# Optimization experiments

Measured on AMD Instinct MI355X. Metric: run time of the kernel, lower is better.

## Reference

```python
import jax, jax.numpy as jnp
import numpy as np

B, DIM, HEADS, HD, H, W = 1, 256, 8, 32, 64, 64
MLP = int(DIM * 4.0)
EPS = 1e-5


def _ln(x, g, b):
    # LayerNorm over channel dim of NCHW (torch applies it on NHWC last dim)
    mu = x.mean(axis=1, keepdims=True)
    var = ((x - mu) ** 2).mean(axis=1, keepdims=True)
    return (x - mu) / jnp.sqrt(var + EPS) * g[None, :, None, None] + b[None, :, None, None]


def _c1(x, w, b):
    # 1x1 conv: w is [out, in]
    return jnp.einsum('bchw,oc->bohw', x, w) + b[None, :, None, None]


def _c3(x, w, b):
    y = jax.lax.conv_general_dilated(x, w, (1, 1), ((1, 1), (1, 1)),
                                     dimension_numbers=('NCHW', 'OIHW', 'NCHW'))
    return y + b[None, :, None, None]


def setup_inputs() -> dict:
    key = jax.random.key(0)
    ks = jax.random.split(key, 16)
    init = lambda k, s: jax.random.normal(k, s, jnp.float32) * 0.02
    d = {}
    d['rgb_feat'] = jax.random.normal(ks[0], (B, DIM, H, W), jnp.float32)
    d['dpt_feat'] = jax.random.normal(ks[1], (B, DIM, H, W), jnp.float32)
    d['x_dpt'] = jax.random.normal(ks[2], (B, 1, 1024, 1024), jnp.float32)
    d['wq'] = init(ks[3], (DIM, DIM)); d['bq'] = jnp.zeros((DIM,), jnp.float32)
    d['wk'] = init(ks[4], (DIM, DIM)); d['bk'] = jnp.zeros((DIM,), jnp.float32)
    d['wv'] = init(ks[5], (DIM, DIM)); d['bv'] = jnp.zeros((DIM,), jnp.float32)
    d['wo'] = init(ks[6], (DIM, DIM)); d['bo'] = jnp.zeros((DIM,), jnp.float32)
    d['g_rgb'] = jnp.ones((DIM,), jnp.float32); d['b_rgb'] = jnp.zeros((DIM,), jnp.float32)
    d['g_dpt'] = jnp.ones((DIM,), jnp.float32); d['b_dpt'] = jnp.zeros((DIM,), jnp.float32)
    d['g1'] = jnp.ones((DIM,), jnp.float32); d['b1'] = jnp.zeros((DIM,), jnp.float32)
    d['g2'] = jnp.ones((DIM,), jnp.float32); d['b2'] = jnp.zeros((DIM,), jnp.float32)
    d['w_mlp1'] = init(ks[7], (MLP, DIM)); d['b_mlp1'] = jnp.zeros((MLP,), jnp.float32)
    d['w_mlp2'] = init(ks[8], (DIM, MLP)); d['b_mlp2'] = jnp.zeros((DIM,), jnp.float32)
    d['w_de1'] = init(ks[9], (DIM, 1, 3, 3)); d['b_de1'] = jnp.zeros((DIM,), jnp.float32)
    d['w_de2'] = init(ks[10], (DIM, DIM)); d['b_de2'] = jnp.zeros((DIM,), jnp.float32)
    d['pos_emb'] = init(ks[11], (1, DIM, 1, 1))
    d['scale'] = jnp.sqrt(jnp.float32(HD))
    return d


def reference(rgb_feat, dpt_feat, x_dpt, wq, bq, wk, bk, wv, bv, wo, bo,
              g_rgb, b_rgb, g_dpt, b_dpt, g1, b1, g2, b2,
              w_mlp1, b_mlp1, w_mlp2, b_mlp2, w_de1, b_de1, w_de2, b_de2,
              pos_emb, scale):
    Bn, C, Hh, Ww = rgb_feat.shape
    n = Hh * Ww
    rgb_ln = _ln(rgb_feat, g_rgb, b_rgb)
    dpt_ln = _ln(dpt_feat, g_dpt, b_dpt)
    # depth positional embedding: bilinear downsample (align_corners=False) + conv3x3 + relu + conv1x1
    xd = jax.image.resize(x_dpt, (Bn, 1, Hh, Ww), method='bilinear', antialias=False)
    pe = _c1(jax.nn.relu(_c3(xd, w_de1, b_de1)), w_de2, b_de2)
    rgb_ln = rgb_ln + pos_emb + pe
    dpt_ln = dpt_ln + pos_emb + pe
    # QKV as [B, heads, head_dim, N]
    q = _c1(rgb_ln, wq, bq).reshape(Bn, HEADS, HD, n)
    k = _c1(dpt_ln, wk, bk).reshape(Bn, HEADS, HD, n)
    v = _c1(dpt_ln, wv, bv).reshape(Bn, HEADS, HD, n)
    scores = jnp.einsum('bhdn,bhdm->bhnm', q, k) / scale
    attn = jax.nn.softmax(scores, axis=-1)  # dropout is identity in eval
    fused = jnp.einsum('bhnm,bhdm->bhdn', attn, v).reshape(Bn, C, Hh, Ww)
    out = _c1(fused, wo, bo) + rgb_feat
    out_ln = _ln(out, g1, b1)
    h = jax.nn.gelu(_c1(out_ln, w_mlp1, b_mlp1), approximate=False)
    mlp_out = _c1(h, w_mlp2, b_mlp2)
    out2 = mlp_out + out_ln
    return _ln(out2, g2, b2)
```

## Files before the change

### kernel.cpp

```cpp
#include <hip/hip_runtime.h>
#include <hip/hip_bf16.h>
#include <math.h>

constexpr int NTOK = 4096;
constexpr int CDIM = 256;
constexpr int MLPD = 1024;
constexpr float EPS_LN = 1e-5f;

typedef __attribute__((ext_vector_type(8))) short bf16x8;
typedef __attribute__((ext_vector_type(4))) float floatx4;
typedef __attribute__((ext_vector_type(16))) float f32x16;
typedef __attribute__((ext_vector_type(2))) unsigned int u32x2;
typedef unsigned short u16;
typedef unsigned int u32;

#if defined(__has_builtin)
#if __has_builtin(__builtin_amdgcn_permlane32_swap)
#define HAVE_PLSWAP 1
#endif
#endif

__device__ __forceinline__ u16 f2bf(float x) {
    union { float f; u32 u; } v; v.f = x;
    u32 r = v.u + 0x7fff + ((v.u >> 16) & 1);
    return (u16)(r >> 16);
}
__device__ __forceinline__ float bf2f(u16 u) {
    union { u32 i; float f; } v; v.i = ((u32)u) << 16; return v.f;
}
__device__ __forceinline__ u32 pkbf(float a, float b) {
    __hip_bfloat162 h = __float22bfloat162_rn(make_float2(a, b));
    union { __hip_bfloat162 h; u32 u; } v; v.h = h; return v.u;
}
__device__ __forceinline__ float gelu_exact(float x) {
    return 0.5f * x * (1.0f + erff(x * 0.70710678118654752f));
}

__global__ __launch_bounds__(256) void k_prep(const float* __restrict__ rgb,
                                              float* __restrict__ rgbT,
                                              const float* __restrict__ dpt,
                                              float* __restrict__ dptT,
                                              const float* __restrict__ xdpt,
                                              const float* __restrict__ w3,
                                              const float* __restrict__ b3,
                                              u16* __restrict__ y,
                                              const float* __restrict__ wq,
                                              const float* __restrict__ wk,
                                              const float* __restrict__ wv,
                                              const float* __restrict__ wo,
                                              const float* __restrict__ wde2,
                                              const float* __restrict__ wm1,
                                              const float* __restrict__ wm2,
                                              u16* __restrict__ arena) {
    int blk = blockIdx.x;
    int t = threadIdx.x;
    if (blk < 512) {
        const float* in = (blk < 256) ? rgb : dpt;
        float* out = (blk < 256) ? rgbT : dptT;
        int tb = blk & 255;
        int c0 = (tb & 63) * 64, r0 = (tb >> 6) * 64;
        __shared__ float T[64][65];
        int rr = t >> 4, cc = (t & 15) * 4;
#pragma unroll
        for (int i = 0; i < 4; ++i) {
            int row = i * 16 + rr;
            float4 v = *(const float4*)(in + (size_t)(r0 + row) * NTOK + c0 + cc);
            T[row][cc] = v.x; T[row][cc + 1] = v.y; T[row][cc + 2] = v.z; T[row][cc + 3] = v.w;
        }
        __syncthreads();
#pragma unroll
        for (int i = 0; i < 4; ++i) {
            int a = i * 16 + rr;
            float4 v;
            v.x = T[cc][a]; v.y = T[cc + 1][a]; v.z = T[cc + 2][a]; v.w = T[cc + 3][a];
            *(float4*)(out + (size_t)(c0 + a) * CDIM + r0 + cc) = v;
        }
    } else if (blk < 768) {
        __shared__ float nb[3][18];
        int n0 = (blk - 512) * 16;
        int yy = n0 >> 6, x0 = n0 & 63;
        if (t < 54) {
            int r = t / 18, cc = t % 18;
            int sy = yy - 1 + r, sx = x0 - 1 + cc;
            float v = 0.f;
            if (sy >= 0 && sy < 64 && sx >= 0 && sx < 64) {
                int r0 = 16 * sy + 7, c0 = 16 * sx + 7;
                v = 0.25f * (xdpt[r0 * 1024 + c0] + xdpt[r0 * 1024 + c0 + 1] +
                             xdpt[(r0 + 1) * 1024 + c0] + xdpt[(r0 + 1) * 1024 + c0 + 1]);
            }
            nb[r][cc] = v;
        }
        __syncthreads();
        float wv9[9];
#pragma unroll
        for (int i = 0; i < 9; ++i) wv9[i] = w3[t * 9 + i];
        float bb = b3[t];
#pragma unroll
        for (int k = 0; k < 16; ++k) {
            float acc = bb;
#pragma unroll
            for (int r = 0; r < 3; ++r)
#pragma unroll
                for (int kx = 0; kx < 3; ++kx) acc += wv9[r * 3 + kx] * nb[r][k + kx];
            y[(size_t)(n0 + k) * CDIM + t] = f2bf(fmaxf(acc, 0.f));
        }
    } else {
        int e0 = (blk - 768) * 1024 + t * 4;
        const float* src; int off;
        if (e0 < 65536)       { src = wq;   off = 0; }
        else if (e0 < 131072) { src = wk;   off = 65536; }
        else if (e0 < 196608) { src = wv;   off = 131072; }
        else if (e0 < 262144) { src = wo;   off = 196608; }
        else if (e0 < 327680) { src = wde2; off = 262144; }
        else if (e0 < 589824) { src = wm1;  off = 327680; }
        else                  { src = wm2;  off = 589824; }
        float4 v = *(const float4*)(src + (e0 - off));
        uint2 o; o.x = pkbf(v.x, v.y); o.y = pkbf(v.z, v.w);
        *(uint2*)(arena + e0) = o;
    }
}

__global__ __launch_bounds__(256) void k_lnT(const void* __restrict__ xA,
                                             const float* __restrict__ gA,
                                             const float* __restrict__ bA,
                                             void* __restrict__ yA,
                                             const void* __restrict__ xB,
                                             const float* __restrict__ gB,
                                             const float* __restrict__ bB,
                                             void* __restrict__ yB,
                                             const u16* __restrict__ pe,
                                             const float* __restrict__ pos,
                                             int xf32) {
    const void* x; const float* g; const float* bb; void* y;
    if (blockIdx.y == 0) { x = xA; g = gA; bb = bA; y = yA; }
    else                 { x = xB; g = gB; bb = bB; y = yB; }
    int n = blockIdx.x * 4 + (threadIdx.x >> 6);
    int lane = threadIdx.x & 63;
    int c = lane * 4;
    float4 xv;
    if (xf32) {
        xv = *((const float4*)x + (size_t)n * 64 + lane);
    } else {
        ushort4 u = *((const ushort4*)x + (size_t)n * 64 + lane);
        xv = make_float4(bf2f(u.x), bf2f(u.y), bf2f(u.z), bf2f(u.w));
    }
    float s = xv.x + xv.y + xv.z + xv.w;
    float s2 = xv.x * xv.x + xv.y * xv.y + xv.z * xv.z + xv.w * xv.w;
#pragma unroll
    for (int off = 1; off < 64; off <<= 1) {
        s += __shfl_xor(s, off, 64);
        s2 += __shfl_xor(s2, off, 64);
    }
    float mu = s * (1.0f / 256.0f);
    float var = s2 * (1.0f / 256.0f) - mu * mu;
    float rsd = rsqrtf(var + EPS_LN);
    float4 g4 = *(const float4*)(g + c);
    float4 b4 = *(const float4*)(bb + c);
    float4 o;
    o.x = (xv.x - mu) * rsd * g4.x + b4.x;
    o.y = (xv.y - mu) * rsd * g4.y + b4.y;
    o.z = (xv.z - mu) * rsd * g4.z + b4.z;
    o.w = (xv.w - mu) * rsd * g4.w + b4.w;
    if (pe) {
        float4 p4 = *(const float4*)(pos + c);
        ushort4 pu = *((const ushort4*)pe + (size_t)n * 64 + lane);
        o.x += p4.x + bf2f(pu.x);
        o.y += p4.y + bf2f(pu.y);
        o.z += p4.z + bf2f(pu.z);
        o.w += p4.w + bf2f(pu.w);
    }
    ushort4 ou;
    ou.x = f2bf(o.x); ou.y = f2bf(o.y); ou.z = f2bf(o.z); ou.w = f2bf(o.w);
    *((ushort4*)y + (size_t)n * 64 + lane) = ou;
}

#define LDB 72
__global__ __launch_bounds__(512) void k_bmm(const u16* __restrict__ X0, const void* __restrict__ W0,
                                             const float* __restrict__ B0, void* __restrict__ Y0, int f0,
                                             const u16* __restrict__ X1, const void* __restrict__ W1,
                                             const float* __restrict__ B1, void* __restrict__ Y1, int f1,
                                             const u16* __restrict__ X2, const void* __restrict__ W2,
                                             const float* __restrict__ B2, void* __restrict__ Y2, int f2,
                                             const void* __restrict__ res, const float* __restrict__ scl,
                                             int M, int K) {
    const u16* X; const void* Wp; const float* bias; void* Yp; int flags;
    if (blockIdx.z == 0)      { X = X0; Wp = W0; bias = B0; Yp = Y0; flags = f0; }
    else if (blockIdx.z == 1) { X = X1; Wp = W1; bias = B1; Yp = Y1; flags = f1; }
    else                      { X = X2; Wp = W2; bias = B2; Yp = Y2; flags = f2; }
    __shared__ u16 Xs[2][64 * LDB];
    __shared__ u16 Ws[2][64 * LDB];
    float* Cred = (float*)&Xs[0][0];

    int tid = threadIdx.x;
    int kg = tid >> 8;
    int t = tid & 255;
    int wid = t >> 6, lane = t & 63;
    int lo16 = lane & 15, quad = lane >> 4;
    int wy = wid & 1, wx = wid >> 1;
    int n0 = blockIdx.x * 64, m0 = blockIdx.y * 64;
    int srow = t >> 2, sseg = t & 3;
    int Khalf = K >> 1;
    int kbase = kg * Khalf;

    floatx4 acc[2][2];
#pragma unroll
    for (int i = 0; i < 2; ++i)
#pragma unroll
        for (int j = 0; j < 2; ++j) acc[i][j] = floatx4{0.f, 0.f, 0.f, 0.f};

    for (int k0 = 0; k0 < Khalf; k0 += 64) {
        int kk = kbase + k0;
        const u16* xp = X + (size_t)(n0 + srow) * K + kk + sseg * 16;
        uint4 xr0 = *(const uint4*)xp;
        uint4 xr1 = *(const uint4*)(xp + 8);
        uint4 wb0, wb1;
        if (flags & 32) {
            const u16* wp = (const u16*)Wp + (size_t)(m0 + srow) * K + kk + sseg * 16;
            wb0 = *(const uint4*)wp;
            wb1 = *(const uint4*)(wp + 8);
        } else {
            const float* wp = (const float*)Wp + (size_t)(m0 + srow) * K + kk + sseg * 16;
            float4 w0 = *(const float4*)wp;
            float4 w1 = *(const float4*)(wp + 4);
            float4 w2 = *(const float4*)(wp + 8);
            float4 w3 = *(const float4*)(wp + 12);
            wb0.x = pkbf(w0.x, w0.y); wb0.y = pkbf(w0.z, w0.w);
            wb0.z = pkbf(w1.x, w1.y); wb0.w = pkbf(w1.z, w1.w);
            wb1.x = pkbf(w2.x, w2.y); wb1.y = pkbf(w2.z, w2.w);
            wb1.z = pkbf(w3.x, w3.y); wb1.w = pkbf(w3.z, w3.w);
        }
        __syncthreads();
        *(uint4*)&Xs[kg][srow * LDB + sseg * 16] = xr0;
        *(uint4*)&Xs[kg][srow * LDB + sseg * 16 + 8] = xr1;
        *(uint4*)&Ws[kg][srow * LDB + sseg * 16] = wb0;
        *(uint4*)&Ws[kg][srow * LDB + sseg * 16 + 8] = wb1;
        __syncthreads();

        const u16* As = (flags & 2) ? &Ws[kg][0] : &Xs[kg][0];
        const u16* Bs = (flags & 2) ? &Xs[kg][0] : &Ws[kg][0];
#pragma unroll
        for (int h = 0; h < 2; ++h) {
            int ko = h * 32 + quad * 8;
            bf16x8 a0 = *(const bf16x8*)&As[(wy * 32 + lo16) * LDB + ko];
            bf16x8 a1 = *(const bf16x8*)&As[(wy * 32 + 16 + lo16) * LDB + ko];
            bf16x8 b0 = *(const bf16x8*)&Bs[(wx * 32 + lo16) * LDB + ko];
            bf16x8 b1 = *(const bf16x8*)&Bs[(wx * 32 + 16 + lo16) * LDB + ko];
            acc[0][0] = __builtin_amdgcn_mfma_f32_16x16x32_bf16(a0, b0, acc[0][0], 0, 0, 0);
            acc[0][1] = __builtin_amdgcn_mfma_f32_16x16x32_bf16(a0, b1, acc[0][1], 0, 0, 0);
            acc[1][0] = __builtin_amdgcn_mfma_f32_16x16x32_bf16(a1, b0, acc[1][0], 0, 0, 0);
            acc[1][1] = __builtin_amdgcn_mfma_f32_16x16x32_bf16(a1, b1, acc[1][1], 0, 0, 0);
        }
    }

    __syncthreads();
    if (kg == 1) {
        float* c = &Cred[t * 17];
#pragma unroll
        for (int i = 0; i < 2; ++i)
#pragma unroll
            for (int j = 0; j < 2; ++j)
#pragma unroll
                for (int r = 0; r < 4; ++r) c[(i * 2 + j) * 4 + r] = acc[i][j][r];
    }
    __syncthreads();
    if (kg == 1) return;
    {
        const float* c = &Cred[t * 17];
#pragma unroll
        for (int i = 0; i < 2; ++i)
#pragma unroll
            for (int j = 0; j < 2; ++j)
#pragma unroll
                for (int r = 0; r < 4; ++r) acc[i][j][r] += c[(i * 2 + j) * 4 + r];
    }

    u16* Y = (u16*)Yp;
    if (flags & 2) {
#pragma unroll
        for (int i = 0; i < 2; ++i)
#pragma unroll
            for (int r = 0; r < 4; ++r) {
                int ch = m0 + wy * 32 + i * 16 + quad * 4 + r;
                float bb = bias[ch];
#pragma unroll
                for (int j = 0; j < 2; ++j) {
                    int tok = n0 + wx * 32 + j * 16 + lo16;
                    Y[(size_t)ch * NTOK + tok] = f2bf(acc[i][j][r] + bb);
                }
            }
    } else {
        float smul = (flags & 16) ? 1.4426950408889634f / scl[0] : 1.0f;
        float bj0 = bias[m0 + wx * 32 + lo16];
        float bj1 = bias[m0 + wx * 32 + 16 + lo16];
        const float* rf = (const float*)res;
        const u16* rb = (const u16*)res;
#pragma unroll
        for (int i = 0; i < 2; ++i)
#pragma unroll
            for (int j = 0; j < 2; ++j) {
                int ch = m0 + wx * 32 + j * 16 + lo16;
                float bb = j ? bj1 : bj0;
#pragma unroll
                for (int r = 0; r < 4; ++r) {
                    int tok = n0 + wy * 32 + i * 16 + quad * 4 + r;
                    float v = (acc[i][j][r] + bb) * smul;
                    if (flags & 1) v = gelu_exact(v);
                    if (flags & 4) v += rf[(size_t)tok * M + ch];
                    if (flags & 8) v += bf2f(rb[(size_t)tok * M + ch]);
                    if (flags & 64)
                        Y[((size_t)(ch >> 5) * NTOK + tok) * 32 + (ch & 31)] = f2bf(v);
                    else
                        Y[(size_t)tok * M + ch] = f2bf(v);
                }
            }
    }
}

#define LDK 40
#define LDV 72
__global__ __launch_bounds__(256) void k_fattn(const u16* __restrict__ Qh,
                                               const u16* __restrict__ Kh,
                                               const u16* __restrict__ Vc,
                                               u16* __restrict__ Op,
                                               float* __restrict__ Lp,
                                               int niter) {
    __shared__ u16 Kt[2][64 * LDK];
    __shared__ u16 Vt[2][32 * LDV];

    int h = blockIdx.y;
    int q0 = blockIdx.x * 128;
    int sp = blockIdx.z;
    int tid = threadIdx.x;
    int wid = tid >> 6, lane = tid & 63;
    int ql = lane & 31, hi = lane >> 5;
    int qtok = q0 + wid * 32 + ql;

    const u16* qp = Qh + ((size_t)h * NTOK + qtok) * 32 + hi * 8;
    bf16x8 bq0 = *(const bf16x8*)(qp);
    bf16x8 bq1 = *(const bf16x8*)(qp + 16);

    int krow = tid >> 2, kseg = tid & 3;
    int vrow = tid >> 3, vseg = tid & 7;
    int kbase = sp * (niter * 64);

    f32x16 oacc = {0.f, 0.f, 0.f, 0.f, 0.f, 0.f, 0.f, 0.f,
                   0.f, 0.f, 0.f, 0.f, 0.f, 0.f, 0.f, 0.f};
    const f32x16 zv = {0.f, 0.f, 0.f, 0.f, 0.f, 0.f, 0.f, 0.f,
                       0.f, 0.f, 0.f, 0.f, 0.f, 0.f, 0.f, 0.f};
    float l = 0.f;

    uint4 kreg = *(const uint4*)(Kh + ((size_t)h * NTOK + kbase + krow) * 32 + kseg * 8);
    uint4 vreg = *(const uint4*)(Vc + (size_t)(h * 32 + vrow) * NTOK + kbase + vseg * 8);

    for (int kt = 0; kt < niter; ++kt) {
        int cb = kt & 1;
        *(uint4*)&Kt[cb][krow * LDK + kseg * 8] = kreg;
        *(uint4*)&Vt[cb][vrow * LDV + vseg * 8] = vreg;
        __syncthreads();
        if (kt + 1 < niter) {
            int kn = kbase + (kt + 1) * 64;
            kreg = *(const uint4*)(Kh + ((size_t)h * NTOK + kn + krow) * 32 + kseg * 8);
            vreg = *(const uint4*)(Vc + (size_t)(h * 32 + vrow) * NTOK + kn + vseg * 8);
        }

#pragma unroll
        for (int sub = 0; sub < 2; ++sub) {
            bf16x8 ak0 = *(const bf16x8*)&Kt[cb][(sub * 32 + ql) * LDK + hi * 8];
            bf16x8 ak1 = *(const bf16x8*)&Kt[cb][(sub * 32 + ql) * LDK + 16 + hi * 8];
            f32x16 s = __builtin_amdgcn_mfma_f32_32x32x16_bf16(ak0, bq0, zv, 0, 0, 0);
            s = __builtin_amdgcn_mfma_f32_32x32x16_bf16(ak1, bq1, s, 0, 0, 0);
            u32 u[8];
#pragma unroll
            for (int t = 0; t < 8; ++t) {
                float pa = __builtin_amdgcn_exp2f(s[2 * t]);
                float pb = __builtin_amdgcn_exp2f(s[2 * t + 1]);
                l += pa + pb;
                u[t] = pkbf(pa, pb);
            }
            uint4 wa, wb;
#ifdef HAVE_PLSWAP
            u32x2 r0 = __builtin_amdgcn_permlane32_swap(u[0], u[2], false, false);
            u32x2 r1 = __builtin_amdgcn_permlane32_swap(u[1], u[3], false, false);
            u32x2 r2 = __builtin_amdgcn_permlane32_swap(u[4], u[6], false, false);
            u32x2 r3 = __builtin_amdgcn_permlane32_swap(u[5], u[7], false, false);
            wa.x = r0[0]; wa.z = r0[1];
            wa.y = r1[0]; wa.w = r1[1];
            wb.x = r2[0]; wb.z = r2[1];
            wb.y = r3[0]; wb.w = r3[1];
#else
            u32 px[8];
#pragma unroll
            for (int t = 0; t < 8; ++t) px[t] = (u32)__shfl_xor((int)u[t], 32, 64);
            wa.x = hi ? px[2] : u[0];
            wa.y = hi ? px[3] : u[1];
            wa.z = hi ? u[2] : px[0];
            wa.w = hi ? u[3] : px[1];
            wb.x = hi ? px[6] : u[4];
            wb.y = hi ? px[7] : u[5];
            wb.z = hi ? u[6] : px[4];
            wb.w = hi ? u[7] : px[5];
#endif
            union { uint4 q; bf16x8 v; } pa0, pa1;
            pa0.q = wa; pa1.q = wb;
            bf16x8 bv0 = *(const bf16x8*)&Vt[cb][ql * LDV + sub * 32 + hi * 8];
            bf16x8 bv1 = *(const bf16x8*)&Vt[cb][ql * LDV + sub * 32 + 16 + hi * 8];
            oacc = __builtin_amdgcn_mfma_f32_32x32x16_bf16(pa0.v, bv0, oacc, 0, 0, 0);
            oacc = __builtin_amdgcn_mfma_f32_32x32x16_bf16(pa1.v, bv1, oacc, 0, 0, 0);
        }
    }

    l += __shfl_xor(l, 32, 64);

    size_t obase = ((size_t)(sp * 8 + h) * NTOK + q0 + wid * 32) * 32 + ql;
#pragma unroll
    for (int r = 0; r < 16; ++r) {
        int qrow = (r & 3) + 8 * (r >> 2) + 4 * hi;
        Op[obase + (size_t)qrow * 32] = f2bf(oacc[r]);
    }
    if (hi == 0) Lp[(size_t)(sp * 8 + h) * NTOK + qtok] = l;
}

__global__ __launch_bounds__(256) void k_comb(const u16* __restrict__ Op,
                                              const float* __restrict__ Lp,
                                              u16* __restrict__ fused,
                                              int split) {
    int n = blockIdx.x * 4 + (threadIdx.x >> 6);
    int lane = threadIdx.x & 63;
    int c = lane * 4;
    int h = c >> 5, d = c & 31;
    float4 o = {0.f, 0.f, 0.f, 0.f};
    float l = 0.f;
    for (int s = 0; s < split; ++s) {
        size_t base = ((size_t)(s * 8 + h) * NTOK + n) * 32 + d;
        uint2 u = *(const uint2*)(Op + base);
        o.x += bf2f((u16)(u.x & 0xffff)); o.y += bf2f((u16)(u.x >> 16));
        o.z += bf2f((u16)(u.y & 0xffff)); o.w += bf2f((u16)(u.y >> 16));
        l += Lp[(size_t)(s * 8 + h) * NTOK + n];
    }
    float inv = 1.0f / l;
    uint2 w;
    w.x = pkbf(o.x * inv, o.y * inv);
    w.y = pkbf(o.z * inv, o.w * inv);
    *(uint2*)(fused + (size_t)n * CDIM + c) = w;
}

__global__ __launch_bounds__(256) void k_lntr(const u16* __restrict__ x,
                                              const float* __restrict__ g,
                                              const float* __restrict__ b,
                                              float* __restrict__ out) {
    __shared__ float T[16][260];
    int n0 = blockIdx.x * 16;
    int t = threadIdx.x;
    int tk = t >> 4, seg = t & 15;
    float v[16];
    {
        const u16* p = x + (size_t)(n0 + tk) * CDIM + seg * 16;
        uint4 a = *(const uint4*)p;
        uint4 bq = *(const uint4*)(p + 8);
        u32 uu[8] = {a.x, a.y, a.z, a.w, bq.x, bq.y, bq.z, bq.w};
#pragma unroll
        for (int i = 0; i < 8; ++i) {
            v[2 * i] = bf2f((u16)(uu[i] & 0xffff));
            v[2 * i + 1] = bf2f((u16)(uu[i] >> 16));
        }
    }
    float s = 0.f, s2 = 0.f;
#pragma unroll
    for (int i = 0; i < 16; ++i) { s += v[i]; s2 += v[i] * v[i]; }
#pragma unroll
    for (int off = 1; off < 16; off <<= 1) {
        s += __shfl_xor(s, off, 64);
        s2 += __shfl_xor(s2, off, 64);
    }
    float mu = s * (1.0f / 256.0f);
    float var = s2 * (1.0f / 256.0f) - mu * mu;
    float rsd = rsqrtf(var + EPS_LN);
#pragma unroll
    for (int i = 0; i < 16; ++i) {
        int c = seg * 16 + i;
        T[tk][c] = (v[i] - mu) * rsd * g[c] + b[c];
    }
    __syncthreads();
    int c = t;
    float o[16];
#pragma unroll
    for (int j = 0; j < 16; ++j) o[j] = T[j][c];
    float* dst = out + (size_t)c * NTOK + n0;
#pragma unroll
    for (int j = 0; j < 4; ++j) {
        float4 w = {o[4 * j], o[4 * j + 1], o[4 * j + 2], o[4 * j + 3]};
        *(float4*)(dst + 4 * j) = w;
    }
}

extern "C" void kernel_launch(void* const* d_in, const int* in_sizes, int n_in,
                              void* d_out, int out_size, void* d_ws, size_t ws_size,
                              hipStream_t stream) {
    const float* rgb    = (const float*)d_in[0];
    const float* dpt    = (const float*)d_in[1];
    const float* x_dpt  = (const float*)d_in[2];
    const float* wq     = (const float*)d_in[3];
    const float* bq     = (const float*)d_in[4];
    const float* wk     = (const float*)d_in[5];
    const float* bk     = (const float*)d_in[6];
    const float* wv     = (const float*)d_in[7];
    const float* bv     = (const float*)d_in[8];
    const float* wo     = (const float*)d_in[9];
    const float* bo     = (const float*)d_in[10];
    const float* g_rgb  = (const float*)d_in[11];
    const float* b_rgb  = (const float*)d_in[12];
    const float* g_dpt  = (const float*)d_in[13];
    const float* b_dpt  = (const float*)d_in[14];
    const float* g1     = (const float*)d_in[15];
    const float* b1     = (const float*)d_in[16];
    const float* g2     = (const float*)d_in[17];
    const float* b2     = (const float*)d_in[18];
    const float* w_mlp1 = (const float*)d_in[19];
    const float* b_mlp1 = (const float*)d_in[20];
    const float* w_mlp2 = (const float*)d_in[21];
    const float* b_mlp2 = (const float*)d_in[22];
    const float* w_de1  = (const float*)d_in[23];
    const float* b_de1  = (const float*)d_in[24];
    const float* w_de2  = (const float*)d_in[25];
    const float* b_de2  = (const float*)d_in[26];
    const float* pos    = (const float*)d_in[27];
    const float* scale  = (const float*)d_in[28];
    float* out = (float*)d_out;

    char* base = (char*)d_ws;
    const size_t MB = 1u << 20;
    float* rgbT    = (float*)(base + 0 * MB);
    float* dptT    = (float*)(base + 4 * MB);
    u16*   outT    = (u16*)(base + 4 * MB);
    float* Lp4     = (float*)(base + 6 * MB);
    u16*   out_lnT = (u16*)(base + 6 * MB);
    u16*   relu3T  = (u16*)(base + 8 * MB);
    u16*   Op4     = (u16*)(base + 8 * MB);
    u16*   hT      = (u16*)(base + 8 * MB);
    u16*   peT     = (u16*)(base + 10 * MB);
    u16*   aqT     = (u16*)(base + 12 * MB);
    u16*   akvT    = (u16*)(base + 14 * MB);
    u16*   Qhm     = (u16*)(base + 16 * MB);
    u16*   out2T   = (u16*)(base + 16 * MB);
    u16*   Khm     = (u16*)(base + 18 * MB);
    u16*   Vcm     = (u16*)(base + 20 * MB);
    u16*   fusedT  = (u16*)(base + 22 * MB);
    u16*   arena   = (u16*)(base + 24 * MB);

    bool aw = ws_size >= 26 * MB;
    int wf = aw ? 32 : 0;
    const void* Wq  = aw ? (const void*)(arena + 0)      : (const void*)wq;
    const void* Wk  = aw ? (const void*)(arena + 65536)  : (const void*)wk;
    const void* Wv  = aw ? (const void*)(arena + 131072) : (const void*)wv;
    const void* Wo  = aw ? (const void*)(arena + 196608) : (const void*)wo;
    const void* Wd2 = aw ? (const void*)(arena + 262144) : (const void*)w_de2;
    const void* Wm1 = aw ? (const void*)(arena + 327680) : (const void*)w_mlp1;
    const void* Wm2 = aw ? (const void*)(arena + 589824) : (const void*)w_mlp2;

    int split = (ws_size >= 68 * MB) ? 8 : 4;
    u16*   Op = (split == 8) ? (u16*)(base + 32 * MB) : Op4;
    float* Lp = (split == 8) ? (float*)(base + 48 * MB) : Lp4;

    k_prep<<<aw ? 512 + 256 + 832 : 512 + 256, 256, 0, stream>>>(
        rgb, rgbT, dpt, dptT, x_dpt, w_de1, b_de1, relu3T,
        wq, wk, wv, wo, w_de2, w_mlp1, w_mlp2, arena);
    k_bmm<<<dim3(64, 4, 1), 512, 0, stream>>>(relu3T, Wd2, b_de2, peT, wf,
                                              nullptr, nullptr, nullptr, nullptr, 0,
                                              nullptr, nullptr, nullptr, nullptr, 0,
                                              nullptr, nullptr, CDIM, CDIM);
    k_lnT<<<dim3(1024, 2), 256, 0, stream>>>(rgbT, g_rgb, b_rgb, aqT,
                                             dptT, g_dpt, b_dpt, akvT,
                                             peT, pos, 1);
    k_bmm<<<dim3(64, 4, 3), 512, 0, stream>>>(aqT, Wq, bq, Qhm, wf | 16 | 64,
                                              akvT, Wk, bk, Khm, wf | 64,
                                              akvT, Wv, bv, Vcm, wf | 2,
                                              nullptr, scale, CDIM, CDIM);
    k_fattn<<<dim3(32, 8, split), 256, 0, stream>>>(Qhm, Khm, Vcm, Op, Lp,
                                                    NTOK / split / 64);
    k_comb<<<1024, 256, 0, stream>>>(Op, Lp, fusedT, split);
    k_bmm<<<dim3(64, 4, 1), 512, 0, stream>>>(fusedT, Wo, bo, outT, wf | 4,
                                              nullptr, nullptr, nullptr, nullptr, 0,
                                              nullptr, nullptr, nullptr, nullptr, 0,
                                              rgbT, nullptr, CDIM, CDIM);
    k_lnT<<<dim3(1024, 1), 256, 0, stream>>>(outT, g1, b1, out_lnT,
                                             nullptr, nullptr, nullptr, nullptr,
                                             nullptr, nullptr, 0);
    k_bmm<<<dim3(64, 16, 1), 512, 0, stream>>>(out_lnT, Wm1, b_mlp1, hT, wf | 1,
                                               nullptr, nullptr, nullptr, nullptr, 0,
                                               nullptr, nullptr, nullptr, nullptr, 0,
                                               nullptr, nullptr, MLPD, CDIM);
    k_bmm<<<dim3(64, 4, 1), 512, 0, stream>>>(hT, Wm2, b_mlp2, out2T, wf | 8,
                                              nullptr, nullptr, nullptr, nullptr, 0,
                                              nullptr, nullptr, nullptr, nullptr, 0,
                                              out_lnT, nullptr, CDIM, MLPD);
    k_lntr<<<256, 256, 0, stream>>>(out2T, g2, b2, out);
}
```

Before: 212.5 us.

## Prefetch GEMM tiles, compute softmax sums via MFMA, fix attention split

The GEMM kernel now loads the next K-tile from global memory into registers while the current tile is consumed, so load latency overlaps with MFMA work. In flash attention, the row-sum of probabilities is computed with extra MFMAs against a ones vector instead of scalar adds plus a cross-lane shuffle, and MFMA sections are wrapped in s_setprio raises. The attention split is pinned to 4 rather than 8 when workspace allows. The trade-offs are more register pressure, extra MFMA work for the sums, sums accumulated from bf16-rounded probabilities, and possibly lower occupancy from the smaller split.

```diff
diff --git a/kernel.cpp b/kernel.cpp
--- a/kernel.cpp
+++ b/kernel.cpp
@@ -208,18 +208,17 @@
 #pragma unroll
         for (int j = 0; j < 2; ++j) acc[i][j] = floatx4{0.f, 0.f, 0.f, 0.f};
 
-    for (int k0 = 0; k0 < Khalf; k0 += 64) {
-        int kk = kbase + k0;
-        const u16* xp = X + (size_t)(n0 + srow) * K + kk + sseg * 16;
-        uint4 xr0 = *(const uint4*)xp;
-        uint4 xr1 = *(const uint4*)(xp + 8);
-        uint4 wb0, wb1;
+    uint4 xr0, xr1, wb0, wb1;
+    {
+        const u16* xp = X + (size_t)(n0 + srow) * K + kbase + sseg * 16;
+        xr0 = *(const uint4*)xp;
+        xr1 = *(const uint4*)(xp + 8);
         if (flags & 32) {
-            const u16* wp = (const u16*)Wp + (size_t)(m0 + srow) * K + kk + sseg * 16;
+            const u16* wp = (const u16*)Wp + (size_t)(m0 + srow) * K + kbase + sseg * 16;
             wb0 = *(const uint4*)wp;
             wb1 = *(const uint4*)(wp + 8);
         } else {
-            const float* wp = (const float*)Wp + (size_t)(m0 + srow) * K + kk + sseg * 16;
+            const float* wp = (const float*)Wp + (size_t)(m0 + srow) * K + kbase + sseg * 16;
             float4 w0 = *(const float4*)wp;
             float4 w1 = *(const float4*)(wp + 4);
             float4 w2 = *(const float4*)(wp + 8);
@@ -229,12 +228,36 @@
             wb1.x = pkbf(w2.x, w2.y); wb1.y = pkbf(w2.z, w2.w);
             wb1.z = pkbf(w3.x, w3.y); wb1.w = pkbf(w3.z, w3.w);
         }
+    }
+
+    for (int k0 = 0; k0 < Khalf; k0 += 64) {
         __syncthreads();
         *(uint4*)&Xs[kg][srow * LDB + sseg * 16] = xr0;
         *(uint4*)&Xs[kg][srow * LDB + sseg * 16 + 8] = xr1;
         *(uint4*)&Ws[kg][srow * LDB + sseg * 16] = wb0;
         *(uint4*)&Ws[kg][srow * LDB + sseg * 16 + 8] = wb1;
         __syncthreads();
+        if (k0 + 64 < Khalf) {
+            int kk = kbase + k0 + 64;
+            const u16* xp = X + (size_t)(n0 + srow) * K + kk + sseg * 16;
+            xr0 = *(const uint4*)xp;
+            xr1 = *(const uint4*)(xp + 8);
+            if (flags & 32) {
+                const u16* wp = (const u16*)Wp + (size_t)(m0 + srow) * K + kk + sseg * 16;
+                wb0 = *(const uint4*)wp;
+                wb1 = *(const uint4*)(wp + 8);
+            } else {
+                const float* wp = (const float*)Wp + (size_t)(m0 + srow) * K + kk + sseg * 16;
+                float4 w0 = *(const float4*)wp;
+                float4 w1 = *(const float4*)(wp + 4);
+                float4 w2 = *(const float4*)(wp + 8);
+                float4 w3 = *(const float4*)(wp + 12);
+                wb0.x = pkbf(w0.x, w0.y); wb0.y = pkbf(w0.z, w0.w);
+                wb0.z = pkbf(w1.x, w1.y); wb0.w = pkbf(w1.z, w1.w);
+                wb1.x = pkbf(w2.x, w2.y); wb1.y = pkbf(w2.z, w2.w);
+                wb1.z = pkbf(w3.x, w3.y); wb1.w = pkbf(w3.z, w3.w);
+            }
+        }
 
         const u16* As = (flags & 2) ? &Ws[kg][0] : &Xs[kg][0];
         const u16* Bs = (flags & 2) ? &Xs[kg][0] : &Ws[kg][0];
@@ -345,9 +368,13 @@
 
     f32x16 oacc = {0.f, 0.f, 0.f, 0.f, 0.f, 0.f, 0.f, 0.f,
                    0.f, 0.f, 0.f, 0.f, 0.f, 0.f, 0.f, 0.f};
+    f32x16 lsum = {0.f, 0.f, 0.f, 0.f, 0.f, 0.f, 0.f, 0.f,
+                   0.f, 0.f, 0.f, 0.f, 0.f, 0.f, 0.f, 0.f};
     const f32x16 zv = {0.f, 0.f, 0.f, 0.f, 0.f, 0.f, 0.f, 0.f,
                        0.f, 0.f, 0.f, 0.f, 0.f, 0.f, 0.f, 0.f};
-    float l = 0.f;
+    union { u32 w[4]; bf16x8 v; } ones;
+    ones.w[0] = 0x3F803F80u; ones.w[1] = 0x3F803F80u;
+    ones.w[2] = 0x3F803F80u; ones.w[3] = 0x3F803F80u;
 
     uint4 kreg = *(const uint4*)(Kh + ((size_t)h * NTOK + kbase + krow) * 32 + kseg * 8);
     uint4 vreg = *(const uint4*)(Vc + (size_t)(h * 32 + vrow) * NTOK + kbase + vseg * 8);
@@ -367,14 +394,15 @@
         for (int sub = 0; sub < 2; ++sub) {
             bf16x8 ak0 = *(const bf16x8*)&Kt[cb][(sub * 32 + ql) * LDK + hi * 8];
             bf16x8 ak1 = *(const bf16x8*)&Kt[cb][(sub * 32 + ql) * LDK + 16 + hi * 8];
+            __builtin_amdgcn_s_setprio(1);
             f32x16 s = __builtin_amdgcn_mfma_f32_32x32x16_bf16(ak0, bq0, zv, 0, 0, 0);
             s = __builtin_amdgcn_mfma_f32_32x32x16_bf16(ak1, bq1, s, 0, 0, 0);
+            __builtin_amdgcn_s_setprio(0);
             u32 u[8];
 #pragma unroll
             for (int t = 0; t < 8; ++t) {
                 float pa = __builtin_amdgcn_exp2f(s[2 * t]);
                 float pb = __builtin_amdgcn_exp2f(s[2 * t + 1]);
-                l += pa + pb;
                 u[t] = pkbf(pa, pb);
             }
             uint4 wa, wb;
@@ -404,12 +432,14 @@
             pa0.q = wa; pa1.q = wb;
             bf16x8 bv0 = *(const bf16x8*)&Vt[cb][ql * LDV + sub * 32 + hi * 8];
             bf16x8 bv1 = *(const bf16x8*)&Vt[cb][ql * LDV + sub * 32 + 16 + hi * 8];
+            __builtin_amdgcn_s_setprio(1);
             oacc = __builtin_amdgcn_mfma_f32_32x32x16_bf16(pa0.v, bv0, oacc, 0, 0, 0);
             oacc = __builtin_amdgcn_mfma_f32_32x32x16_bf16(pa1.v, bv1, oacc, 0, 0, 0);
-        }
-    }
-
-    l += __shfl_xor(l, 32, 64);
+            lsum = __builtin_amdgcn_mfma_f32_32x32x16_bf16(pa0.v, ones.v, lsum, 0, 0, 0);
+            lsum = __builtin_amdgcn_mfma_f32_32x32x16_bf16(pa1.v, ones.v, lsum, 0, 0, 0);
+            __builtin_amdgcn_s_setprio(0);
+        }
+    }
 
     size_t obase = ((size_t)(sp * 8 + h) * NTOK + q0 + wid * 32) * 32 + ql;
 #pragma unroll
@@ -417,7 +447,14 @@
         int qrow = (r & 3) + 8 * (r >> 2) + 4 * hi;
         Op[obase + (size_t)qrow * 32] = f2bf(oacc[r]);
     }
-    if (hi == 0) Lp[(size_t)(sp * 8 + h) * NTOK + qtok] = l;
+    if (ql == 0) {
+        size_t lb = (size_t)(sp * 8 + h) * NTOK + q0 + wid * 32;
+#pragma unroll
+        for (int r = 0; r < 16; ++r) {
+            int qrow = (r & 3) + 8 * (r >> 2) + 4 * hi;
+            Lp[lb + qrow] = lsum[r];
+        }
+    }
 }
 
 __global__ __launch_bounds__(256) void k_comb(const u16* __restrict__ Op,
@@ -532,10 +569,10 @@
     float* rgbT    = (float*)(base + 0 * MB);
     float* dptT    = (float*)(base + 4 * MB);
     u16*   outT    = (u16*)(base + 4 * MB);
-    float* Lp4     = (float*)(base + 6 * MB);
+    float* Lp      = (float*)(base + 6 * MB);
     u16*   out_lnT = (u16*)(base + 6 * MB);
     u16*   relu3T  = (u16*)(base + 8 * MB);
-    u16*   Op4     = (u16*)(base + 8 * MB);
+    u16*   Op      = (u16*)(base + 8 * MB);
     u16*   hT      = (u16*)(base + 8 * MB);
     u16*   peT     = (u16*)(base + 10 * MB);
     u16*   aqT     = (u16*)(base + 12 * MB);
@@ -557,9 +594,7 @@
     const void* Wm1 = aw ? (const void*)(arena + 327680) : (const void*)w_mlp1;
     const void* Wm2 = aw ? (const void*)(arena + 589824) : (const void*)w_mlp2;
 
-    int split = (ws_size >= 68 * MB) ? 8 : 4;
-    u16*   Op = (split == 8) ? (u16*)(base + 32 * MB) : Op4;
-    float* Lp = (split == 8) ? (float*)(base + 48 * MB) : Lp4;
+    const int split = 4;
 
     k_prep<<<aw ? 512 + 256 + 832 : 512 + 256, 256, 0, stream>>>(
         rgb, rgbT, dpt, dptT, x_dpt, w_de1, b_de1, relu3T,
```

Measured after the change: 214.6 us. No clear change (+1.0%).
